# Kernel optimization log

Measured on AMD Instinct MI355X. Metric: run time of the kernel, lower is better.

The kernel has to match this reference:

```python
import jax, jax.numpy as jnp
import numpy as np

B, DIN, D, F, NH, HD, OUT = 8192, 4096, 512, 2048, 3, 256, 896  # OUT = chunk_len*action_hidden_dim*grid = 8*16*7
EPS = 1e-5

def _ln(x, g, b):
    m = jnp.mean(x, -1, keepdims=True)
    v = jnp.mean((x - m) ** 2, -1, keepdims=True)
    return (x - m) * jax.lax.rsqrt(v + EPS) * g + b

def setup_inputs() -> dict:
    key = jax.random.key(0)
    ks = list(jax.random.split(key, 16))
    r = lambda k, shape: jax.random.normal(k, shape, jnp.float32) * 0.02
    return dict(
        x=jax.random.normal(ks[0], (B, DIN), jnp.float32),
        w_in=r(ks[1], (DIN, D)), b_in=jnp.zeros((D,), jnp.float32),
        pos=r(ks[2], (D,)),  # position_encoding[:, 0, :] (seq_len is always 1)
        ln1_g=jnp.ones((D,), jnp.float32), ln1_b=jnp.zeros((D,), jnp.float32),
        wv_sa=r(ks[3], (D, D)), bv_sa=jnp.zeros((D,), jnp.float32),
        wo_sa=r(ks[4], (D, D)), bo_sa=jnp.zeros((D,), jnp.float32),
        ln2_g=jnp.ones((D,), jnp.float32), ln2_b=jnp.zeros((D,), jnp.float32),
        wv_ca=r(ks[5], (D, D)), bv_ca=jnp.zeros((D,), jnp.float32),
        wo_ca=r(ks[6], (D, D)), bo_ca=jnp.zeros((D,), jnp.float32),
        ln3_g=jnp.ones((D,), jnp.float32), ln3_b=jnp.zeros((D,), jnp.float32),
        w_ff1=r(ks[7], (D, F)), b_ff1=jnp.zeros((F,), jnp.float32),
        w_ff2=r(ks[8], (F, D)), b_ff2=jnp.zeros((D,), jnp.float32),
        lnout_g=jnp.ones((D,), jnp.float32), lnout_b=jnp.zeros((D,), jnp.float32),
        wh1=r(ks[9], (NH, D, HD)), bh1=jnp.zeros((NH, HD), jnp.float32),
        lnh_g=jnp.ones((NH, HD), jnp.float32), lnh_b=jnp.zeros((NH, HD), jnp.float32),
        wh2=r(ks[10], (NH, HD, OUT)), bh2=jnp.zeros((NH, OUT), jnp.float32),
    )

def reference(x, w_in, b_in, pos, ln1_g, ln1_b, wv_sa, bv_sa, wo_sa, bo_sa,
              ln2_g, ln2_b, wv_ca, bv_ca, wo_ca, bo_ca, ln3_g, ln3_b,
              w_ff1, b_ff1, w_ff2, b_ff2, lnout_g, lnout_b,
              wh1, bh1, lnh_g, lnh_b, wh2, bh2):
    # input projection + position encoding (seq_len = 1 -> pos[0])
    h = x @ w_in + b_in + pos          # [B, D]
    mem = h
    # norm_first TransformerDecoderLayer with seq_len=1: softmax weights == 1,
    # so attention = out_proj(V(.)) exactly; Q/K and norm2 have no effect.
    h = h + (_ln(h, ln1_g, ln1_b) @ wv_sa + bv_sa) @ wo_sa + bo_sa      # self-attn block
    h = h + (mem @ wv_ca + bv_ca) @ wo_ca + bo_ca                       # cross-attn block (memory = tgt)
    h = h + jax.nn.gelu(_ln(h, ln3_g, ln3_b) @ w_ff1 + b_ff1, approximate=False) @ w_ff2 + b_ff2
    h = _ln(h, lnout_g, lnout_b)                                        # decoder output_norm
    # three classification heads, batched over head dim
    z = jnp.einsum('bd,hdk->bhk', h, wh1) + bh1                         # [B, 3, 256]
    z = _ln(jax.nn.gelu(z, approximate=False), lnh_g, lnh_b)
    logits = jnp.einsum('bhk,hko->bho', z, wh2) + bh2                   # [B, 3, 896]
    return logits.reshape(x.shape[0], NH, 128, 7)                       # [B, 3, chunk*act_hid, grid]
```

## Files before the change

### kernel.cpp

```cpp
#include <hip/hip_runtime.h>
#include <math.h>


typedef unsigned short u16;
typedef __attribute__((ext_vector_type(8))) short bf16x8;
typedef __attribute__((ext_vector_type(4))) float f32x4;
typedef __attribute__((ext_vector_type(8))) unsigned short u16x8;
typedef __attribute__((ext_vector_type(4))) unsigned short u16x4;

__device__ __forceinline__ float bf2f(u16 u){
    union { unsigned int i; float f; } x; x.i = ((unsigned int)u) << 16; return x.f;
}
__device__ __forceinline__ u16 f2bf(float f){
    union { float f; unsigned int i; } x; x.f = f;
    unsigned int r = x.i + 0x7fffu + ((x.i >> 16) & 1u);
    return (u16)(r >> 16);
}
__device__ __forceinline__ float gelu_fast(float v){
    const float u = 1.5957691216f * v * (1.0f + 0.044715f * v * v);
    const float e = __expf(u);
    return v * (1.0f - 1.0f / (e + 1.0f));
}
#define GLOAD16(src, dst) __builtin_amdgcn_global_load_lds( \
    (const __attribute__((address_space(1))) void*)(src),   \
    (__attribute__((address_space(3))) void*)(dst), 16, 0, 0)
#define SCHED0 __builtin_amdgcn_sched_barrier(0)

template<bool GELU, bool RES, bool AF32, bool OUTF32, bool PART>
__global__ __launch_bounds__(256) void gemm64(
    const void* __restrict__ A, const void* __restrict__ A2, int ksplit,
    const u16* __restrict__ Bt, const float* __restrict__ bias,
    const u16* __restrict__ res, int ldr,
    void* __restrict__ Cout, int K, int lda, int ldb, int ldc,
    long azs, long bzs, int biaszs, long czs, int kch)
{
    __shared__ __align__(16) u16 As[2][64 * 64];
    __shared__ __align__(16) u16 Bs[2][128 * 64];
    const int tid = threadIdx.x;
    const int w = tid >> 6, l = tid & 63;
    const int wr = w >> 1, wc = w & 1;
    const int m0 = blockIdx.x * 64, n0 = blockIdx.y * 128;
    const int z = blockIdx.z;
    int kbeg = 0, kend = K;
    if (PART) { kbeg = z * kch; kend = min(kbeg + kch, K); }
    const u16* A16 = (const u16*)A + (PART ? 0 : (size_t)z * azs);
    const float* Af = (const float*)A;
    const u16* BtZ = Bt + (PART ? 0 : (size_t)z * bzs);
    const int swc = (l & 7) ^ (l >> 3);

    f32x4 acc[2][4];
#pragma unroll
    for (int i = 0; i < 2; ++i)
#pragma unroll
        for (int j = 0; j < 4; ++j) acc[i][j] = (f32x4){0.f, 0.f, 0.f, 0.f};

    auto stageB = [&](int buf, int k0) {
#pragma unroll
        for (int j = 0; j < 4; ++j) {
            const int rb = w * 32 + j * 8;
            const u16* gb = BtZ + (size_t)(n0 + rb + (l >> 3)) * ldb + k0 + swc * 8;
            GLOAD16(gb, &Bs[buf][rb * 64]);
        }
    };
    auto stageA16 = [&](int buf, int k0) {
        const u16* base = (k0 >= ksplit) ? ((const u16*)A2 + (k0 - ksplit)) : (A16 + k0);
#pragma unroll
        for (int j = 0; j < 2; ++j) {
            const int rb = w * 16 + j * 8;
            const u16* ga = base + (size_t)(m0 + rb + (l >> 3)) * lda + swc * 8;
            GLOAD16(ga, &As[buf][rb * 64]);
        }
    };
    auto loadA = [&](int k0, float4& p0, float4& p1, float4& p2, float4& p3) {
        const float* g = Af + (size_t)(m0 + (tid >> 2)) * lda + k0 + (tid & 3) * 16;
        p0 = *(const float4*)g;       p1 = *(const float4*)(g + 4);
        p2 = *(const float4*)(g + 8); p3 = *(const float4*)(g + 12);
    };
    auto writeA = [&](const float4& p0, const float4& p1, const float4& p2,
                      const float4& p3, int buf) {
        const int row = tid >> 2, c0 = (tid & 3) * 2;
        u16x8 v0, v1;
        v0[0] = f2bf(p0.x); v0[1] = f2bf(p0.y); v0[2] = f2bf(p0.z); v0[3] = f2bf(p0.w);
        v0[4] = f2bf(p1.x); v0[5] = f2bf(p1.y); v0[6] = f2bf(p1.z); v0[7] = f2bf(p1.w);
        v1[0] = f2bf(p2.x); v1[1] = f2bf(p2.y); v1[2] = f2bf(p2.z); v1[3] = f2bf(p2.w);
        v1[4] = f2bf(p3.x); v1[5] = f2bf(p3.y); v1[6] = f2bf(p3.z); v1[7] = f2bf(p3.w);
        *(u16x8*)&As[buf][row * 64 + ((c0)     ^ (row & 7)) * 8] = v0;
        *(u16x8*)&As[buf][row * 64 + ((c0 + 1) ^ (row & 7)) * 8] = v1;
    };
    int cur = 0;
    auto compute = [&]() {
#pragma unroll
        for (int kk = 0; kk < 2; ++kk) {
            const int kcb = kk * 4 + (l >> 4);
            bf16x8 a[2], b[4];
#pragma unroll
            for (int i = 0; i < 2; ++i) {
                const int row = wr * 32 + i * 16 + (l & 15);
                a[i] = *(const bf16x8*)&As[cur][row * 64 + (kcb ^ (l & 7)) * 8];
            }
#pragma unroll
            for (int j = 0; j < 4; ++j) {
                const int row = wc * 64 + j * 16 + (l & 15);
                b[j] = *(const bf16x8*)&Bs[cur][row * 64 + (kcb ^ (l & 7)) * 8];
            }
#pragma unroll
            for (int i = 0; i < 2; ++i)
#pragma unroll
                for (int j = 0; j < 4; ++j)
                    acc[i][j] = __builtin_amdgcn_mfma_f32_16x16x32_bf16(a[i], b[j], acc[i][j], 0, 0, 0);
        }
    };

    const int nt = (kend - kbeg) >> 6;
    if (AF32) {
        float4 a0, a1, a2, a3, b0, b1, b2, b3;
        loadA(kbeg, a0, a1, a2, a3);
        stageB(0, kbeg);
        if (nt > 1) {
            loadA(kbeg + 64, b0, b1, b2, b3);
            asm volatile("s_waitcnt vmcnt(4)" ::: "memory");
        } else {
            asm volatile("s_waitcnt vmcnt(0)" ::: "memory");
        }
        writeA(a0, a1, a2, a3, 0);
        asm volatile("s_waitcnt lgkmcnt(0)" ::: "memory");
        auto stepA = [&](int t, float4& w0, float4& w1, float4& w2, float4& w3,
                         float4& l0, float4& l1, float4& l2, float4& l3) {
            const bool ldA = (t + 2) < nt;
            const bool stB = (t + 1) < nt;
            if (ldA) loadA(kbeg + ((t + 2) << 6), l0, l1, l2, l3);
            if (stB) stageB(cur ^ 1, kbeg + ((t + 1) << 6));
            if (ldA)      asm volatile("s_waitcnt vmcnt(8)" ::: "memory");
            else if (stB) asm volatile("s_waitcnt vmcnt(4)" ::: "memory");
            else          asm volatile("s_waitcnt vmcnt(0)" ::: "memory");
            SCHED0;
            __builtin_amdgcn_s_barrier();
            SCHED0;
            compute();
            if (stB) writeA(w0, w1, w2, w3, cur ^ 1);
            asm volatile("s_waitcnt lgkmcnt(0)" ::: "memory");
            SCHED0;
            __builtin_amdgcn_s_barrier();
            SCHED0;
            cur ^= 1;
        };
        int t = 0;
        while (t + 2 <= nt) {
            stepA(t,     b0, b1, b2, b3, a0, a1, a2, a3);
            stepA(t + 1, a0, a1, a2, a3, b0, b1, b2, b3);
            t += 2;
        }
        if (t < nt) stepA(t, b0, b1, b2, b3, a0, a1, a2, a3);
    } else {
        stageA16(0, kbeg);
        stageB(0, kbeg);
        for (int t = 0; t < nt; ++t) {
            const bool more = (t + 1) < nt;
            if (more) {
                const int kn = kbeg + ((t + 1) << 6);
                stageA16(cur ^ 1, kn);
                stageB(cur ^ 1, kn);
            }
            if (more) asm volatile("s_waitcnt vmcnt(6)" ::: "memory");
            else      asm volatile("s_waitcnt vmcnt(0)" ::: "memory");
            SCHED0;
            __builtin_amdgcn_s_barrier();
            SCHED0;
            compute();
            asm volatile("" ::: "memory");
            SCHED0;
            __builtin_amdgcn_s_barrier();
            SCHED0;
            cur ^= 1;
        }
    }

    float* cF = (float*)Cout + (size_t)z * czs;
    u16*   cH = (u16*)Cout + (size_t)z * czs;
    const float* biasZ = (!PART && bias) ? bias + (size_t)z * biaszs : nullptr;
#pragma unroll
    for (int i = 0; i < 2; ++i) {
#pragma unroll
        for (int j = 0; j < 4; ++j) {
            const int col = n0 + wc * 64 + j * 16 + (l & 15);
            const int rowb = m0 + wr * 32 + i * 16 + (l >> 4) * 4;
#pragma unroll
            for (int r = 0; r < 4; ++r) {
                const int row = rowb + r;
                float v = acc[i][j][r];
                if (PART) {
                    cF[(size_t)row * ldc + col] = v;
                } else {
                    if (biasZ) v += biasZ[col];
                    if (RES) v += bf2f(res[(size_t)row * ldr + col]);
                    if (GELU) v = gelu_fast(v);
                    if (OUTF32) cF[(size_t)row * ldc + col] = v;
                    else        cH[(size_t)row * ldc + col] = f2bf(v);
                }
            }
        }
    }
}

template<int NP, bool RES, bool WRITEH>
__global__ __launch_bounds__(256) void reduceLN512(
    const float* __restrict__ part, long pzs, const float* __restrict__ bias,
    const u16* __restrict__ res, const float* __restrict__ g,
    const float* __restrict__ b, u16* __restrict__ outH, u16* __restrict__ outT)
{
    const int wid = threadIdx.x >> 6, l = threadIdx.x & 63;
    const size_t row = (size_t)blockIdx.x * 4 + wid;
    const size_t base = row * 512 + l * 8;
    float f[8];
    {
        const float4 p0 = *(const float4*)(part + base);
        const float4 p1 = *(const float4*)(part + base + 4);
        f[0]=p0.x; f[1]=p0.y; f[2]=p0.z; f[3]=p0.w;
        f[4]=p1.x; f[5]=p1.y; f[6]=p1.z; f[7]=p1.w;
    }
#pragma unroll
    for (int p = 1; p < NP; ++p) {
        const float4 p0 = *(const float4*)(part + (size_t)p * pzs + base);
        const float4 p1 = *(const float4*)(part + (size_t)p * pzs + base + 4);
        f[0]+=p0.x; f[1]+=p0.y; f[2]+=p0.z; f[3]+=p0.w;
        f[4]+=p1.x; f[5]+=p1.y; f[6]+=p1.z; f[7]+=p1.w;
    }
    {
        const float4 b0 = *(const float4*)(bias + l * 8);
        const float4 b1 = *(const float4*)(bias + l * 8 + 4);
        f[0]+=b0.x; f[1]+=b0.y; f[2]+=b0.z; f[3]+=b0.w;
        f[4]+=b1.x; f[5]+=b1.y; f[6]+=b1.z; f[7]+=b1.w;
    }
    if (RES) {
        const u16x8 r = *(const u16x8*)(res + base);
#pragma unroll
        for (int j = 0; j < 8; ++j) f[j] += bf2f(r[j]);
    }
    if (WRITEH) {
        u16x8 h;
#pragma unroll
        for (int j = 0; j < 8; ++j) h[j] = f2bf(f[j]);
        *(u16x8*)(outH + base) = h;
    }
    float s = 0.f, q = 0.f;
#pragma unroll
    for (int j = 0; j < 8; ++j) { s += f[j]; q += f[j] * f[j]; }
#pragma unroll
    for (int o = 32; o > 0; o >>= 1) { s += __shfl_xor(s, o); q += __shfl_xor(q, o); }
    const float mean = s * (1.f / 512.f);
    const float var = q * (1.f / 512.f) - mean * mean;
    const float rstd = rsqrtf(var + 1e-5f);
    u16x8 t;
#pragma unroll
    for (int j = 0; j < 8; ++j) {
        const int c = l * 8 + j;
        t[j] = f2bf((f[j] - mean) * rstd * g[c] + b[c]);
    }
    *(u16x8*)(outT + base) = t;
}

__global__ __launch_bounds__(256) void lnh_kernel(
    const u16* __restrict__ in, const float* __restrict__ g,
    const float* __restrict__ b, u16* __restrict__ out)
{
    const int wid = threadIdx.x >> 6, l = threadIdx.x & 63;
    const int unit = blockIdx.x * 4 + wid;
    const int h = unit >> 13, row = unit & 8191;
    const size_t base = (size_t)row * 768 + h * 256 + l * 4;
    u16x4 v = *(const u16x4*)(in + base);
    float f[4], s = 0.f, q = 0.f;
#pragma unroll
    for (int j = 0; j < 4; ++j) { f[j] = bf2f(v[j]); s += f[j]; q += f[j] * f[j]; }
#pragma unroll
    for (int o = 32; o > 0; o >>= 1) { s += __shfl_xor(s, o); q += __shfl_xor(q, o); }
    const float mean = s * (1.f / 256.f);
    const float var = q * (1.f / 256.f) - mean * mean;
    const float rstd = rsqrtf(var + 1e-5f);
    u16x4 ov;
#pragma unroll
    for (int j = 0; j < 4; ++j) {
        const int c = h * 256 + l * 4 + j;
        ov[j] = f2bf((f[j] - mean) * rstd * g[c] + b[c]);
    }
    *(u16x4*)(out + base) = ov;
}

struct PrepPtrs {
    const float *w_in, *w_ff1, *w_ff2, *wo_ca, *wo_sa, *wv_ca, *wv_sa;
    const float *wh1, *wh2, *b_in, *pos, *bv_sa, *bo_sa, *bv_ca, *bo_ca;
    u16 *w_inT, *wff1t, *wff2t, *woT2, *wv2b, *Wh1t, *Wh2t;
    float *bias_in, *b_comb;
};

__device__ __forceinline__ void dev_transpose(
    const float* in, u16* out, int K, int N, int t, int tid, u16 (*tile)[33])
{
    const int nt = N >> 5;
    const int n0 = (t % nt) * 32, k0 = (t / nt) * 32;
    const int tx = tid & 31, ty = tid >> 5;
#pragma unroll
    for (int i = 0; i < 32; i += 8)
        tile[ty + i][tx] = f2bf(in[(size_t)(k0 + ty + i) * N + (n0 + tx)]);
    __syncthreads();
#pragma unroll
    for (int i = 0; i < 32; i += 8)
        out[(size_t)(n0 + ty + i) * K + (k0 + tx)] = tile[tx][ty + i];
}

__global__ __launch_bounds__(256) void prep_all(PrepPtrs p)
{
    __shared__ u16 tile[32][33];
    __shared__ float psa[4][64], pca[4][64];
    const int tid = threadIdx.x;
    int b = blockIdx.x;
    if (b < 2048) { dev_transpose(p.w_in, p.w_inT, 4096, 512, b, tid, tile); return; }
    b -= 2048;
    if (b < 1024) { dev_transpose(p.w_ff1, p.wff1t, 512, 2048, b, tid, tile); return; }
    b -= 1024;
    if (b < 1024) { dev_transpose(p.w_ff2, p.wff2t, 2048, 512, b, tid, tile); return; }
    b -= 1024;
    if (b < 256) { dev_transpose(p.wo_ca, p.woT2, 512, 512, b, tid, tile); return; }
    b -= 256;
    if (b < 256) { dev_transpose(p.wo_sa, p.woT2 + 512 * 512, 512, 512, b, tid, tile); return; }
    b -= 256;
    if (b < 1536) {
        const int idx = b * 256 + tid;
        const int d = idx & 511, j = idx >> 9;
        const int h = j >> 8, kk = j & 255;
        p.Wh1t[idx] = f2bf(p.wh1[((size_t)(h * 512 + d)) * 256 + kk]);
        return;
    }
    b -= 1536;
    if (b < 2688) {
        const int idx = b * 256 + tid;
        const int kk = idx & 255, t = idx >> 8;
        const int h = t / 896, o = t - h * 896;
        p.Wh2t[idx] = f2bf(p.wh2[((size_t)(h * 256 + kk)) * 896 + o]);
        return;
    }
    b -= 2688;
    if (b < 256) {
        const float* src = (b < 128) ? p.wv_ca : p.wv_sa;
        u16* dst = p.wv2b + (b < 128 ? 0 : 512 * 512);
        const int i = (b & 127) * 256 + tid;
        const float4* q = (const float4*)src + (size_t)i * 2;
        const float4 a = q[0], c = q[1];
        u16x8 v;
        v[0] = f2bf(a.x); v[1] = f2bf(a.y); v[2] = f2bf(a.z); v[3] = f2bf(a.w);
        v[4] = f2bf(c.x); v[5] = f2bf(c.y); v[6] = f2bf(c.z); v[7] = f2bf(c.w);
        *(u16x8*)(dst + (size_t)i * 8) = v;
        return;
    }
    b -= 256;
    {
        const int ii = tid & 63, kg = tid >> 6;
        const int i = b * 64 + ii;
        float sa = 0.f, ca = 0.f;
        for (int k = kg; k < 512; k += 4) {
            sa += p.bv_sa[k] * p.wo_sa[(size_t)k * 512 + i];
            ca += p.bv_ca[k] * p.wo_ca[(size_t)k * 512 + i];
        }
        psa[kg][ii] = sa; pca[kg][ii] = ca;
        __syncthreads();
        if (kg == 0) {
            p.bias_in[i] = p.b_in[i] + p.pos[i];
            p.b_comb[i] = psa[0][ii] + psa[1][ii] + psa[2][ii] + psa[3][ii]
                        + pca[0][ii] + pca[1][ii] + pca[2][ii] + pca[3][ii]
                        + p.bo_sa[i] + p.bo_ca[i];
        }
    }
}

extern "C" void kernel_launch(void* const* d_in, const int* in_sizes, int n_in,
                              void* d_out, int out_size, void* d_ws, size_t ws_size,
                              hipStream_t stream)
{
    const float* x      = (const float*)d_in[0];
    const float* ln1_g  = (const float*)d_in[4];
    const float* ln1_b  = (const float*)d_in[5];
    const float* ln3_g  = (const float*)d_in[16];
    const float* ln3_b  = (const float*)d_in[17];
    const float* b_ff1  = (const float*)d_in[19];
    const float* b_ff2  = (const float*)d_in[21];
    const float* lnoutg = (const float*)d_in[22];
    const float* lnoutb = (const float*)d_in[23];
    const float* bh1    = (const float*)d_in[25];
    const float* lnh_g  = (const float*)d_in[26];
    const float* lnh_b  = (const float*)d_in[27];
    const float* bh2    = (const float*)d_in[29];
    float* out = (float*)d_out;
    const int KBIG = 0x7fffffff;

    char* wsp = (char*)d_ws;
    size_t off = 0;
    auto ALLOC = [&](size_t n) { char* r = wsp + off; off = (off + n + 255) & ~(size_t)255; return r; };
    u16* w_inT  = (u16*)ALLOC(512UL * 4096 * 2);
    u16* wff1t  = (u16*)ALLOC(2048UL * 512 * 2);
    u16* wff2t  = (u16*)ALLOC(512UL * 2048 * 2);
    u16* woT2   = (u16*)ALLOC(2UL * 512 * 512 * 2);
    u16* wv2b   = (u16*)ALLOC(2UL * 512 * 512 * 2);
    u16* Wct    = (u16*)ALLOC(512UL * 1024 * 2);
    u16* Wh1t   = (u16*)ALLOC(768UL * 512 * 2);
    u16* Wh2t   = (u16*)ALLOC(3UL * 896 * 256 * 2);
    float* bias_in = (float*)ALLOC(512 * 4);
    float* b_comb  = (float*)ALLOC(512 * 4);
    u16* h0   = (u16*)ALLOC(8192UL * 512 * 2);
    u16* T    = (u16*)ALLOC(8192UL * 512 * 2);
    u16* hbuf = (u16*)ALLOC(8192UL * 512 * 2);
    u16* G    = (u16*)ALLOC(8192UL * 2048 * 2);
    u16* Z  = G;
    u16* Z2 = (u16*)((char*)G + 8192UL * 768 * 2);
    float* partO = out;
    const long PZS = 8192L * 512;

    PrepPtrs pp;
    pp.w_in = (const float*)d_in[1];  pp.w_ff1 = (const float*)d_in[18];
    pp.w_ff2 = (const float*)d_in[20];
    pp.wo_ca = (const float*)d_in[14]; pp.wo_sa = (const float*)d_in[8];
    pp.wv_ca = (const float*)d_in[12]; pp.wv_sa = (const float*)d_in[6];
    pp.wh1 = (const float*)d_in[24];   pp.wh2 = (const float*)d_in[28];
    pp.b_in = (const float*)d_in[2];   pp.pos = (const float*)d_in[3];
    pp.bv_sa = (const float*)d_in[7];  pp.bo_sa = (const float*)d_in[9];
    pp.bv_ca = (const float*)d_in[13]; pp.bo_ca = (const float*)d_in[15];
    pp.w_inT = w_inT; pp.wff1t = wff1t; pp.wff2t = wff2t;
    pp.woT2 = woT2; pp.wv2b = wv2b; pp.Wh1t = Wh1t; pp.Wh2t = Wh2t;
    pp.bias_in = bias_in; pp.b_comb = b_comb;
    prep_all<<<9096, 256, 0, stream>>>(pp);
    gemm64<false, false, false, false, false><<<dim3(8, 4, 2), 256, 0, stream>>>(
        woT2, nullptr, KBIG, wv2b, nullptr, nullptr, 0, Wct,
        512, 512, 512, 1024, 512 * 512, 512 * 512, 0, 512, 0);

    gemm64<false, false, true, false, true><<<dim3(128, 4, 3), 256, 0, stream>>>(
        x, nullptr, KBIG, w_inT, nullptr, nullptr, 0, partO,
        4096, 4096, 4096, 512, 0, 0, 0, PZS, 1408);
    reduceLN512<3, false, true><<<2048, 256, 0, stream>>>(
        partO, PZS, bias_in, nullptr, ln1_g, ln1_b, h0, T);
    gemm64<false, false, false, false, true><<<dim3(128, 4, 2), 256, 0, stream>>>(
        h0, T, 512, Wct, nullptr, nullptr, 0, partO,
        1024, 512, 1024, 512, 0, 0, 0, PZS, 512);
    reduceLN512<2, true, true><<<2048, 256, 0, stream>>>(
        partO, PZS, b_comb, h0, ln3_g, ln3_b, hbuf, T);
    gemm64<true, false, false, false, false><<<dim3(128, 16), 256, 0, stream>>>(
        T, nullptr, KBIG, wff1t, b_ff1, nullptr, 0, G,
        512, 512, 512, 2048, 0, 0, 0, 0, 0);
    gemm64<false, false, false, false, true><<<dim3(128, 4, 2), 256, 0, stream>>>(
        G, nullptr, KBIG, wff2t, nullptr, nullptr, 0, partO,
        2048, 2048, 2048, 512, 0, 0, 0, PZS, 1024);
    reduceLN512<2, true, false><<<2048, 256, 0, stream>>>(
        partO, PZS, b_ff2, hbuf, lnoutg, lnoutb, nullptr, T);
    gemm64<true, false, false, false, false><<<dim3(128, 6), 256, 0, stream>>>(
        T, nullptr, KBIG, Wh1t, bh1, nullptr, 0, Z,
        512, 512, 512, 768, 0, 0, 0, 0, 0);
    lnh_kernel<<<6144, 256, 0, stream>>>(Z, lnh_g, lnh_b, Z2);
    gemm64<false, false, false, true, false><<<dim3(128, 7, 3), 256, 0, stream>>>(
        Z2, nullptr, KBIG, Wh2t, bh2, nullptr, 0, out,
        256, 768, 256, 2688, 256, 896 * 256, 896, 896, 0);
}
```

Baseline: 338.8 us.

## Pre-convert x to bf16 in prep kernel and drop fp32-A GEMM path

Adds a bf16 conversion of the 8192x4096 input x to the prep kernel, storing it in the output buffer as scratch. The input-projection GEMM then uses the bf16 async global-to-LDS load path instead of loading fp32 A through registers and converting inside the loop. Its split-K goes from 3 to 2 and partials now go into the G workspace, so the reduce sums two slices. This simplifies the GEMM pipeline but adds a separate read of x and a write of the bf16 copy.

```diff
diff --git a/kernel.cpp b/kernel.cpp
--- a/kernel.cpp
+++ b/kernel.cpp
@@ -26,9 +26,9 @@
     (__attribute__((address_space(3))) void*)(dst), 16, 0, 0)
 #define SCHED0 __builtin_amdgcn_sched_barrier(0)
 
-template<bool GELU, bool RES, bool AF32, bool OUTF32, bool PART>
+template<bool GELU, bool RES, bool OUTF32, bool PART>
 __global__ __launch_bounds__(256) void gemm64(
-    const void* __restrict__ A, const void* __restrict__ A2, int ksplit,
+    const u16* __restrict__ A, const u16* __restrict__ A2, int ksplit,
     const u16* __restrict__ Bt, const float* __restrict__ bias,
     const u16* __restrict__ res, int ldr,
     void* __restrict__ Cout, int K, int lda, int ldb, int ldc,
@@ -43,8 +43,7 @@
     const int z = blockIdx.z;
     int kbeg = 0, kend = K;
     if (PART) { kbeg = z * kch; kend = min(kbeg + kch, K); }
-    const u16* A16 = (const u16*)A + (PART ? 0 : (size_t)z * azs);
-    const float* Af = (const float*)A;
+    const u16* A16 = A + (PART ? 0 : (size_t)z * azs);
     const u16* BtZ = Bt + (PART ? 0 : (size_t)z * bzs);
     const int swc = (l & 7) ^ (l >> 3);
 
@@ -63,7 +62,7 @@
         }
     };
     auto stageA16 = [&](int buf, int k0) {
-        const u16* base = (k0 >= ksplit) ? ((const u16*)A2 + (k0 - ksplit)) : (A16 + k0);
+        const u16* base = (k0 >= ksplit) ? (A2 + (k0 - ksplit)) : (A16 + k0);
 #pragma unroll
         for (int j = 0; j < 2; ++j) {
             const int rb = w * 16 + j * 8;
@@ -71,22 +70,6 @@
             GLOAD16(ga, &As[buf][rb * 64]);
         }
     };
-    auto loadA = [&](int k0, float4& p0, float4& p1, float4& p2, float4& p3) {
-        const float* g = Af + (size_t)(m0 + (tid >> 2)) * lda + k0 + (tid & 3) * 16;
-        p0 = *(const float4*)g;       p1 = *(const float4*)(g + 4);
-        p2 = *(const float4*)(g + 8); p3 = *(const float4*)(g + 12);
-    };
-    auto writeA = [&](const float4& p0, const float4& p1, const float4& p2,
-                      const float4& p3, int buf) {
-        const int row = tid >> 2, c0 = (tid & 3) * 2;
-        u16x8 v0, v1;
-        v0[0] = f2bf(p0.x); v0[1] = f2bf(p0.y); v0[2] = f2bf(p0.z); v0[3] = f2bf(p0.w);
-        v0[4] = f2bf(p1.x); v0[5] = f2bf(p1.y); v0[6] = f2bf(p1.z); v0[7] = f2bf(p1.w);
-        v1[0] = f2bf(p2.x); v1[1] = f2bf(p2.y); v1[2] = f2bf(p2.z); v1[3] = f2bf(p2.w);
-        v1[4] = f2bf(p3.x); v1[5] = f2bf(p3.y); v1[6] = f2bf(p3.z); v1[7] = f2bf(p3.w);
-        *(u16x8*)&As[buf][row * 64 + ((c0)     ^ (row & 7)) * 8] = v0;
-        *(u16x8*)&As[buf][row * 64 + ((c0 + 1) ^ (row & 7)) * 8] = v1;
-    };
     int cur = 0;
     auto compute = [&]() {
 #pragma unroll
@@ -112,67 +95,26 @@
     };
 
     const int nt = (kend - kbeg) >> 6;
-    if (AF32) {
-        float4 a0, a1, a2, a3, b0, b1, b2, b3;
-        loadA(kbeg, a0, a1, a2, a3);
-        stageB(0, kbeg);
-        if (nt > 1) {
-            loadA(kbeg + 64, b0, b1, b2, b3);
-            asm volatile("s_waitcnt vmcnt(4)" ::: "memory");
-        } else {
-            asm volatile("s_waitcnt vmcnt(0)" ::: "memory");
-        }
-        writeA(a0, a1, a2, a3, 0);
-        asm volatile("s_waitcnt lgkmcnt(0)" ::: "memory");
-        auto stepA = [&](int t, float4& w0, float4& w1, float4& w2, float4& w3,
-                         float4& l0, float4& l1, float4& l2, float4& l3) {
-            const bool ldA = (t + 2) < nt;
-            const bool stB = (t + 1) < nt;
-            if (ldA) loadA(kbeg + ((t + 2) << 6), l0, l1, l2, l3);
-            if (stB) stageB(cur ^ 1, kbeg + ((t + 1) << 6));
-            if (ldA)      asm volatile("s_waitcnt vmcnt(8)" ::: "memory");
-            else if (stB) asm volatile("s_waitcnt vmcnt(4)" ::: "memory");
-            else          asm volatile("s_waitcnt vmcnt(0)" ::: "memory");
-            SCHED0;
-            __builtin_amdgcn_s_barrier();
-            SCHED0;
-            compute();
-            if (stB) writeA(w0, w1, w2, w3, cur ^ 1);
-            asm volatile("s_waitcnt lgkmcnt(0)" ::: "memory");
-            SCHED0;
-            __builtin_amdgcn_s_barrier();
-            SCHED0;
-            cur ^= 1;
-        };
-        int t = 0;
-        while (t + 2 <= nt) {
-            stepA(t,     b0, b1, b2, b3, a0, a1, a2, a3);
-            stepA(t + 1, a0, a1, a2, a3, b0, b1, b2, b3);
-            t += 2;
-        }
-        if (t < nt) stepA(t, b0, b1, b2, b3, a0, a1, a2, a3);
-    } else {
-        stageA16(0, kbeg);
-        stageB(0, kbeg);
-        for (int t = 0; t < nt; ++t) {
-            const bool more = (t + 1) < nt;
-            if (more) {
-                const int kn = kbeg + ((t + 1) << 6);
-                stageA16(cur ^ 1, kn);
-                stageB(cur ^ 1, kn);
-            }
-            if (more) asm volatile("s_waitcnt vmcnt(6)" ::: "memory");
-            else      asm volatile("s_waitcnt vmcnt(0)" ::: "memory");
-            SCHED0;
-            __builtin_amdgcn_s_barrier();
-            SCHED0;
-            compute();
-            asm volatile("" ::: "memory");
-            SCHED0;
-            __builtin_amdgcn_s_barrier();
-            SCHED0;
-            cur ^= 1;
-        }
+    stageA16(0, kbeg);
+    stageB(0, kbeg);
+    for (int t = 0; t < nt; ++t) {
+        const bool more = (t + 1) < nt;
+        if (more) {
+            const int kn = kbeg + ((t + 1) << 6);
+            stageA16(cur ^ 1, kn);
+            stageB(cur ^ 1, kn);
+        }
+        if (more) asm volatile("s_waitcnt vmcnt(6)" ::: "memory");
+        else      asm volatile("s_waitcnt vmcnt(0)" ::: "memory");
+        SCHED0;
+        __builtin_amdgcn_s_barrier();
+        SCHED0;
+        compute();
+        asm volatile("" ::: "memory");
+        SCHED0;
+        __builtin_amdgcn_s_barrier();
+        SCHED0;
+        cur ^= 1;
     }
 
     float* cF = (float*)Cout + (size_t)z * czs;
@@ -286,11 +228,21 @@
 }
 
 struct PrepPtrs {
-    const float *w_in, *w_ff1, *w_ff2, *wo_ca, *wo_sa, *wv_ca, *wv_sa;
+    const float *x, *w_in, *w_ff1, *w_ff2, *wo_ca, *wo_sa, *wv_ca, *wv_sa;
     const float *wh1, *wh2, *b_in, *pos, *bv_sa, *bo_sa, *bv_ca, *bo_ca;
-    u16 *w_inT, *wff1t, *wff2t, *woT2, *wv2b, *Wh1t, *Wh2t;
+    u16 *xbf, *w_inT, *wff1t, *wff2t, *woT2, *wv2b, *Wh1t, *Wh2t;
     float *bias_in, *b_comb;
 };
+
+__device__ __forceinline__ void dev_cvt8(const float* src, u16* dst, int i)
+{
+    const float4* q = (const float4*)src + (size_t)i * 2;
+    const float4 a = q[0], c = q[1];
+    u16x8 v;
+    v[0] = f2bf(a.x); v[1] = f2bf(a.y); v[2] = f2bf(a.z); v[3] = f2bf(a.w);
+    v[4] = f2bf(c.x); v[5] = f2bf(c.y); v[6] = f2bf(c.z); v[7] = f2bf(c.w);
+    *(u16x8*)(dst + (size_t)i * 8) = v;
+}
 
 __device__ __forceinline__ void dev_transpose(
     const float* in, u16* out, int K, int N, int t, int tid, u16 (*tile)[33])
@@ -313,6 +265,8 @@
     __shared__ float psa[4][64], pca[4][64];
     const int tid = threadIdx.x;
     int b = blockIdx.x;
+    if (b < 16384) { dev_cvt8(p.x, p.xbf, b * 256 + tid); return; }
+    b -= 16384;
     if (b < 2048) { dev_transpose(p.w_in, p.w_inT, 4096, 512, b, tid, tile); return; }
     b -= 2048;
     if (b < 1024) { dev_transpose(p.w_ff1, p.wff1t, 512, 2048, b, tid, tile); return; }
@@ -340,15 +294,8 @@
     }
     b -= 2688;
     if (b < 256) {
-        const float* src = (b < 128) ? p.wv_ca : p.wv_sa;
-        u16* dst = p.wv2b + (b < 128 ? 0 : 512 * 512);
-        const int i = (b & 127) * 256 + tid;
-        const float4* q = (const float4*)src + (size_t)i * 2;
-        const float4 a = q[0], c = q[1];
-        u16x8 v;
-        v[0] = f2bf(a.x); v[1] = f2bf(a.y); v[2] = f2bf(a.z); v[3] = f2bf(a.w);
-        v[4] = f2bf(c.x); v[5] = f2bf(c.y); v[6] = f2bf(c.z); v[7] = f2bf(c.w);
-        *(u16x8*)(dst + (size_t)i * 8) = v;
+        if (b < 128) dev_cvt8(p.wv_ca, p.wv2b, b * 256 + tid);
+        else         dev_cvt8(p.wv_sa, p.wv2b + 512 * 512, (b - 128) * 256 + tid);
         return;
     }
     b -= 256;
@@ -375,7 +322,6 @@
                               void* d_out, int out_size, void* d_ws, size_t ws_size,
                               hipStream_t stream)
 {
-    const float* x      = (const float*)d_in[0];
     const float* ln1_g  = (const float*)d_in[4];
     const float* ln1_b  = (const float*)d_in[5];
     const float* ln3_g  = (const float*)d_in[16];
@@ -410,10 +356,13 @@
     u16* G    = (u16*)ALLOC(8192UL * 2048 * 2);
     u16* Z  = G;
     u16* Z2 = (u16*)((char*)G + 8192UL * 768 * 2);
+    u16*   xbf   = (u16*)d_out;
+    float* partG = (float*)G;
     float* partO = out;
     const long PZS = 8192L * 512;
 
     PrepPtrs pp;
+    pp.x = (const float*)d_in[0];
     pp.w_in = (const float*)d_in[1];  pp.w_ff1 = (const float*)d_in[18];
     pp.w_ff2 = (const float*)d_in[20];
     pp.wo_ca = (const float*)d_in[14]; pp.wo_sa = (const float*)d_in[8];
@@ -422,37 +371,38 @@
     pp.b_in = (const float*)d_in[2];   pp.pos = (const float*)d_in[3];
     pp.bv_sa = (const float*)d_in[7];  pp.bo_sa = (const float*)d_in[9];
     pp.bv_ca = (const float*)d_in[13]; pp.bo_ca = (const float*)d_in[15];
+    pp.xbf = xbf;
     pp.w_inT = w_inT; pp.wff1t = wff1t; pp.wff2t = wff2t;
     pp.woT2 = woT2; pp.wv2b = wv2b; pp.Wh1t = Wh1t; pp.Wh2t = Wh2t;
     pp.bias_in = bias_in; pp.b_comb = b_comb;
-    prep_all<<<9096, 256, 0, stream>>>(pp);
-    gemm64<false, false, false, false, false><<<dim3(8, 4, 2), 256, 0, stream>>>(
+    prep_all<<<25480, 256, 0, stream>>>(pp);
+    gemm64<false, false, false, false><<<dim3(8, 4, 2), 256, 0, stream>>>(
         woT2, nullptr, KBIG, wv2b, nullptr, nullptr, 0, Wct,
         512, 512, 512, 1024, 512 * 512, 512 * 512, 0, 512, 0);
 
-    gemm64<false, false, true, false, true><<<dim3(128, 4, 3), 256, 0, stream>>>(
-        x, nullptr, KBIG, w_inT, nullptr, nullptr, 0, partO,
-        4096, 4096, 4096, 512, 0, 0, 0, PZS, 1408);
-    reduceLN512<3, false, true><<<2048, 256, 0, stream>>>(
-        partO, PZS, bias_in, nullptr, ln1_g, ln1_b, h0, T);
-    gemm64<false, false, false, false, true><<<dim3(128, 4, 2), 256, 0, stream>>>(
-        h0, T, 512, Wct, nullptr, nullptr, 0, partO,
+    gemm64<false, false, false, true><<<dim3(128, 4, 2), 256, 0, stream>>>(
+        xbf, nullptr, KBIG, w_inT, nullptr, nullptr, 0, partG,
+        4096, 4096, 4096, 512, 0, 0, 0, PZS, 2048);
+    reduceLN512<2, false, true><<<2048, 256, 0, stream>>>(
+        partG, PZS, bias_in, nullptr, ln1_g, ln1_b, h0, T);
+    gemm64<false, false, false, true><<<dim3(128, 4, 2), 256, 0, stream>>>(
+        h0, T, 512, Wct, nullptr, nullptr, 0, partG,
         1024, 512, 1024, 512, 0, 0, 0, PZS, 512);
     reduceLN512<2, true, true><<<2048, 256, 0, stream>>>(
-        partO, PZS, b_comb, h0, ln3_g, ln3_b, hbuf, T);
-    gemm64<true, false, false, false, false><<<dim3(128, 16), 256, 0, stream>>>(
+        partG, PZS, b_comb, h0, ln3_g, ln3_b, hbuf, T);
+    gemm64<true, false, false, false><<<dim3(128, 16), 256, 0, stream>>>(
         T, nullptr, KBIG, wff1t, b_ff1, nullptr, 0, G,
         512, 512, 512, 2048, 0, 0, 0, 0, 0);
-    gemm64<false, false, false, false, true><<<dim3(128, 4, 2), 256, 0, stream>>>(
+    gemm64<false, false, false, true><<<dim3(128, 4, 2), 256, 0, stream>>>(
         G, nullptr, KBIG, wff2t, nullptr, nullptr, 0, partO,
         2048, 2048, 2048, 512, 0, 0, 0, PZS, 1024);
     reduceLN512<2, true, false><<<2048, 256, 0, stream>>>(
         partO, PZS, b_ff2, hbuf, lnoutg, lnoutb, nullptr, T);
-    gemm64<true, false, false, false, false><<<dim3(128, 6), 256, 0, stream>>>(
+    gemm64<true, false, false, false><<<dim3(128, 6), 256, 0, stream>>>(
         T, nullptr, KBIG, Wh1t, bh1, nullptr, 0, Z,
         512, 512, 512, 768, 0, 0, 0, 0, 0);
     lnh_kernel<<<6144, 256, 0, stream>>>(Z, lnh_g, lnh_b, Z2);
-    gemm64<false, false, false, true, false><<<dim3(128, 7, 3), 256, 0, stream>>>(
+    gemm64<false, false, true, false><<<dim3(128, 7, 3), 256, 0, stream>>>(
         Z2, nullptr, KBIG, Wh2t, bh2, nullptr, 0, out,
         256, 768, 256, 2688, 256, 896 * 256, 896, 896, 0);
 }
```

Result: no change. 333.5 us (-1.6%).
